# Kernel optimization log

Measured on AMD Instinct MI355X. Metric: run time of the kernel, lower is better.

## Reference

```python
import jax, jax.numpy as jnp
import numpy as np

EPS = 1e-5


def _layer(x, g, b, W_in, b_in, W_h, b_h, W_out, b_out):
    # x: [B, T, D]
    mu = jnp.mean(x, axis=-1, keepdims=True)
    var = jnp.mean(jnp.square(x - mu), axis=-1, keepdims=True)
    x_n = (x - mu) * jax.lax.rsqrt(var + EPS) * g + b
    # in_proj for all timesteps at once (same math as per-step linear)
    uv = jnp.einsum('btd,ed->bte', x_n, W_in) + b_in  # [B, T, 2D]
    d = x.shape[-1]
    u = jnp.transpose(uv[..., :d], (1, 0, 2))  # [T, B, D]
    v = jnp.transpose(uv[..., d:], (1, 0, 2))  # [T, B, D]

    def step(h, uv_t):
        u_t, v_t = uv_t
        gate = jax.nn.sigmoid(u_t)
        cand = jnp.tanh(v_t + h @ W_h.T + b_h)
        h_new = gate * cand + (1.0 - gate) * h
        y = h_new @ W_out.T + b_out
        return h_new, y

    h0 = jnp.zeros((x.shape[0], d), dtype=x.dtype)
    _, ys = jax.lax.scan(step, h0, (u, v))  # ys: [T, B, D]
    return x + jnp.transpose(ys, (1, 0, 2))


def setup_inputs() -> dict:
    key = jax.random.key(0)
    B, T, D, L = 8, 2048, 1024, 2
    ks = jax.random.split(key, 8)
    s = 1.0 / np.sqrt(D)
    return {
        'x': jax.random.normal(ks[0], (B, T, D), dtype=jnp.float32),
        'ln_g': jnp.ones((L, D), dtype=jnp.float32),
        'ln_b': jnp.zeros((L, D), dtype=jnp.float32),
        'W_in': jax.random.normal(ks[1], (L, 2 * D, D), dtype=jnp.float32) * s,
        'b_in': jnp.zeros((L, 2 * D), dtype=jnp.float32),
        'W_h': jax.random.normal(ks[2], (L, D, D), dtype=jnp.float32) * s,
        'b_h': jnp.zeros((L, D), dtype=jnp.float32),
        'W_out': jax.random.normal(ks[3], (L, D, D), dtype=jnp.float32) * s,
        'b_out': jnp.zeros((L, D), dtype=jnp.float32),
    }


def reference(x, ln_g, ln_b, W_in, b_in, W_h, b_h, W_out, b_out):
    out = x
    for l in range(W_in.shape[0]):  # small fixed n_layers loop
        out = _layer(out, ln_g[l], ln_b[l], W_in[l], b_in[l], W_h[l], b_h[l],
                     W_out[l], b_out[l])
    return out
```

## Files before the change

kernel.cpp:

```cpp
#include <hip/hip_runtime.h>
#include <stdint.h>
#include <stddef.h>

typedef __bf16 bf16;
typedef __bf16 bf16x8 __attribute__((ext_vector_type(8)));
typedef __bf16 bf16x4 __attribute__((ext_vector_type(4)));
typedef float  f32x4  __attribute__((ext_vector_type(4)));

#define B_ 8
#define T_ 2048
#define D_ 1024
#define L_ 2

#define AS1C(p) ((const __attribute__((address_space(1))) void*)(p))
#define AS3(p)  ((__attribute__((address_space(3))) void*)(p))


__global__ __launch_bounds__(256) void cvt_kernel(const float* __restrict__ in,
                                                  bf16* __restrict__ out, int n4) {
  int i = blockIdx.x * 256 + threadIdx.x;
  if (i >= n4) return;
  float4 v = ((const float4*)in)[i];
  bf16x4 o = { (bf16)v.x, (bf16)v.y, (bf16)v.z, (bf16)v.w };
  ((bf16x4*)out)[i] = o;
}

__global__ __launch_bounds__(256) void ln_kernel(const float* __restrict__ x,
                                                 const float* __restrict__ g,
                                                 const float* __restrict__ b,
                                                 bf16* __restrict__ xn) {
  const int row = blockIdx.x;
  const int tid = threadIdx.x;
  const float4 v = ((const float4*)(x + (size_t)row * D_))[tid];
  float s1 = v.x + v.y + v.z + v.w;
  float s2 = v.x * v.x + v.y * v.y + v.z * v.z + v.w * v.w;
#pragma unroll
  for (int off = 1; off < 64; off <<= 1) {
    s1 += __shfl_xor(s1, off);
    s2 += __shfl_xor(s2, off);
  }
  __shared__ float r1[4], r2[4];
  if ((tid & 63) == 0) { r1[tid >> 6] = s1; r2[tid >> 6] = s2; }
  __syncthreads();
  s1 = r1[0] + r1[1] + r1[2] + r1[3];
  s2 = r2[0] + r2[1] + r2[2] + r2[3];
  const float mu = s1 * (1.f / D_);
  const float var = s2 * (1.f / D_) - mu * mu;
  const float rs = rsqrtf(var + 1e-5f);
  const float4 gv = ((const float4*)g)[tid];
  const float4 bv = ((const float4*)b)[tid];
  bf16x4 o = { (bf16)((v.x - mu) * rs * gv.x + bv.x),
               (bf16)((v.y - mu) * rs * gv.y + bv.y),
               (bf16)((v.z - mu) * rs * gv.z + bv.z),
               (bf16)((v.w - mu) * rs * gv.w + bv.w) };
  ((bf16x4*)(xn + (size_t)row * D_))[tid] = o;
}

__global__ __launch_bounds__(256) void prep2_kernel(const float* __restrict__ Win2,
    const float* __restrict__ g2, const float* __restrict__ be2,
    const float* __restrict__ bin2, bf16* __restrict__ W2p,
    float* __restrict__ csum, float* __restrict__ cbias) {
  const int n = blockIdx.x;
  const int tid = threadIdx.x;
  const float4 w4 = ((const float4*)(Win2 + (size_t)n * 1024))[tid];
  const float4 g4 = ((const float4*)g2)[tid];
  const float4 b4 = ((const float4*)be2)[tid];
  bf16x4 o = { (bf16)(g4.x * w4.x), (bf16)(g4.y * w4.y),
               (bf16)(g4.z * w4.z), (bf16)(g4.w * w4.w) };
  ((bf16x4*)(W2p + (size_t)n * 1024))[tid] = o;
  float s = (float)o[0] + (float)o[1] + (float)o[2] + (float)o[3];
  float cbv = b4.x * w4.x + b4.y * w4.y + b4.z * w4.z + b4.w * w4.w;
#pragma unroll
  for (int off = 1; off < 64; off <<= 1) {
    s += __shfl_xor(s, off);
    cbv += __shfl_xor(cbv, off);
  }
  __shared__ float rs_[4], rc_[4];
  if ((tid & 63) == 0) { rs_[tid >> 6] = s; rc_[tid >> 6] = cbv; }
  __syncthreads();
  if (tid == 0) {
    csum[n] = rs_[0] + rs_[1] + rs_[2] + rs_[3];
    cbias[n] = rc_[0] + rc_[1] + rc_[2] + rc_[3] + bin2[n];
  }
}

__global__ __launch_bounds__(256) void gemm_uv(const bf16* __restrict__ A,
                                               const bf16* __restrict__ Bw,
                                               const float* __restrict__ bias,
                                               bf16* __restrict__ uvp,
                                               int M, int N, int K) {
  __shared__ bf16 As[128 * 32];
  __shared__ bf16 Bs[128 * 32];
  const int tid = threadIdx.x;
  const int lane = tid & 63;
  const int wave = tid >> 6;
  const int m0 = blockIdx.y * 128;
  const int n0 = blockIdx.x * 128;
  const int wm = (wave >> 1) * 64;
  const int wn = (wave & 1) * 64;
  f32x4 acc[4][4] = {};

  for (int kt = 0; kt < K; kt += 32) {
#pragma unroll
    for (int it = 0; it < 2; ++it) {
      const int gidx = it * 256 + tid;
      const int row = gidx >> 2;
      const int col = (gidx & 3) << 3;
      __builtin_amdgcn_global_load_lds(AS1C(A + (size_t)(m0 + row) * K + kt + col),
                                       AS3(&As[gidx * 8]), 16, 0, 0);
      __builtin_amdgcn_global_load_lds(AS1C(Bw + (size_t)(n0 + row) * K + kt + col),
                                       AS3(&Bs[gidx * 8]), 16, 0, 0);
    }
    __syncthreads();
    bf16x8 af[4], bfr[4];
#pragma unroll
    for (int i = 0; i < 4; ++i)
      af[i] = *(const bf16x8*)&As[(wm + i * 16 + (lane & 15)) * 32 + (lane >> 4) * 8];
#pragma unroll
    for (int j = 0; j < 4; ++j)
      bfr[j] = *(const bf16x8*)&Bs[(wn + j * 16 + (lane & 15)) * 32 + (lane >> 4) * 8];
#pragma unroll
    for (int i = 0; i < 4; ++i)
#pragma unroll
      for (int j = 0; j < 4; ++j)
        acc[i][j] = __builtin_amdgcn_mfma_f32_16x16x32_bf16(af[i], bfr[j], acc[i][j], 0, 0, 0);
    __syncthreads();
  }

  const int cr = (lane >> 4) * 4;
  const int cc = lane & 15;
#pragma unroll
  for (int i = 0; i < 4; ++i) {
#pragma unroll
    for (int j = 0; j < 4; ++j) {
      const int mb = m0 + wm + i * 16 + cr;
      const int n = n0 + wn + j * 16 + cc;
      const float bn = bias[n];
      const int p = n >> 10;
      const int nn2 = n & 1023;
#pragma unroll
      for (int r = 0; r < 4; ++r) {
        const int row = mb + r;
        const int b = row >> 11;
        const int t = row & (T_ - 1);
        uvp[(size_t)p * T_ * 8192 + (size_t)t * 8192 + nn2 * 8 + b] =
            (bf16)(acc[i][j][r] + bn);
      }
    }
  }
}

__global__ __launch_bounds__(256) void gemm_hfrag(const char* __restrict__ Hb,
                                                  const bf16* __restrict__ Bw,
                                                  const float* __restrict__ bias,
                                                  const char* __restrict__ residF,
                                                  float* __restrict__ C,
                                                  int M, int N, int K) {
  __shared__ bf16 As[128 * 32];
  __shared__ bf16 Bs[128 * 32];
  const int tid = threadIdx.x;
  const int lane = tid & 63;
  const int wave = tid >> 6;
  const int m0 = blockIdx.y * 128;
  const int n0 = blockIdx.x * 128;
  const int wm = (wave >> 1) * 64;
  const int wn = (wave & 1) * 64;
  f32x4 acc[4][4] = {};

  for (int kt = 0; kt < K; kt += 32) {
#pragma unroll
    for (int it = 0; it < 2; ++it) {
      const int g = it * 256 + tid;
      const int r = g >> 2;
      const int sub = g & 3;
      const int R = m0 + r;
      const int bb = R >> 11;
      const int tt = R & (T_ - 1);
      const char* src = Hb + (size_t)tt * 16384 + (size_t)(kt >> 5) * 512
                        + (sub * 8 + bb) * 16;
      __builtin_amdgcn_global_load_lds(AS1C(src), AS3(&As[g * 8]), 16, 0, 0);
      __builtin_amdgcn_global_load_lds(AS1C(Bw + (size_t)(n0 + r) * K + kt + (sub << 3)),
                                       AS3(&Bs[g * 8]), 16, 0, 0);
    }
    __syncthreads();
    bf16x8 af[4], bfr[4];
#pragma unroll
    for (int i = 0; i < 4; ++i)
      af[i] = *(const bf16x8*)&As[(wm + i * 16 + (lane & 15)) * 32 + (lane >> 4) * 8];
#pragma unroll
    for (int j = 0; j < 4; ++j)
      bfr[j] = *(const bf16x8*)&Bs[(wn + j * 16 + (lane & 15)) * 32 + (lane >> 4) * 8];
#pragma unroll
    for (int i = 0; i < 4; ++i)
#pragma unroll
      for (int j = 0; j < 4; ++j)
        acc[i][j] = __builtin_amdgcn_mfma_f32_16x16x32_bf16(af[i], bfr[j], acc[i][j], 0, 0, 0);
    __syncthreads();
  }

  const int cr = (lane >> 4) * 4;
  const int cc = lane & 15;
#pragma unroll
  for (int i = 0; i < 4; ++i) {
#pragma unroll
    for (int j = 0; j < 4; ++j) {
      const int mb = m0 + wm + i * 16 + cr;
      const int n = n0 + wn + j * 16 + cc;
      const float bn = bias[n];
      const int foffn = (n >> 5) * 512 + (((n & 31) >> 3) * 8) * 16 + (n & 7) * 2;
#pragma unroll
      for (int r = 0; r < 4; ++r) {
        const int row = mb + r;
        const int b = row >> 11;
        const int tt2 = row & (T_ - 1);
        const float resid =
            (float)*(const bf16*)(residF + (size_t)tt2 * 16384 + foffn + b * 16);
        C[(size_t)row * N + n] = acc[i][j][r] + bn + resid;
      }
    }
  }
}

__device__ __forceinline__ void load_wb(bf16x8 (&wB)[32], const bf16* Wrow) {
  const int half = ((threadIdx.x & 63) >> 4) << 3;
#pragma unroll
  for (int kk = 0; kk < 32; ++kk)
    wB[kk] = *(const bf16x8*)(Wrow + kk * 32 + half);
#pragma unroll
  for (int kk = 0; kk < 32; ++kk)
    asm volatile("" : "+a"(wB[kk]));
}

__device__ __forceinline__ f32x4 frag_matvec(const char* __restrict__ dF, int rdoff,
                                             const bf16x8 (&wB)[32]) {
  f32x4 a0 = {0.f, 0.f, 0.f, 0.f}, a1 = a0, a2 = a0, a3 = a0;
#pragma unroll
  for (int kk = 0; kk < 32; kk += 4) {
    bf16x8 f0 = *(const bf16x8*)(dF + kk * 512 + rdoff);
    bf16x8 f1 = *(const bf16x8*)(dF + (kk + 1) * 512 + rdoff);
    bf16x8 f2 = *(const bf16x8*)(dF + (kk + 2) * 512 + rdoff);
    bf16x8 f3 = *(const bf16x8*)(dF + (kk + 3) * 512 + rdoff);
    a0 = __builtin_amdgcn_mfma_f32_16x16x32_bf16(f0, wB[kk], a0, 0, 0, 0);
    a1 = __builtin_amdgcn_mfma_f32_16x16x32_bf16(f1, wB[kk + 1], a1, 0, 0, 0);
    a2 = __builtin_amdgcn_mfma_f32_16x16x32_bf16(f2, wB[kk + 2], a2, 0, 0, 0);
    a3 = __builtin_amdgcn_mfma_f32_16x16x32_bf16(f3, wB[kk + 3], a3, 0, 0, 0);
  }
  return (a0 + a1) + (a2 + a3);
}

template <int SLP>
__device__ __forceinline__ void poll8(const unsigned* base, unsigned tgt) {
  const int lane = threadIdx.x & 63;
  unsigned sv = tgt;
  if (lane < 8)
    sv = __hip_atomic_load(base + lane * 16, __ATOMIC_RELAXED, __HIP_MEMORY_SCOPE_AGENT);
  while (!__all((int)(sv >= tgt))) {
    __builtin_amdgcn_s_sleep(SLP);
    if (lane < 8)
      sv = __hip_atomic_load(base + lane * 16, __ATOMIC_RELAXED, __HIP_MEMORY_SCOPE_AGENT);
  }
  (void)__hip_atomic_load(base, __ATOMIC_ACQUIRE, __HIP_MEMORY_SCOPE_AGENT);
}

__device__ __forceinline__ void poll2s3(const unsigned* sync, int wg, unsigned tgt) {
  const int lane = threadIdx.x & 63;
  unsigned sv = tgt;
  if (lane < 2)
    sv = __hip_atomic_load(sync + 256 + ((lane ? 8 : 0) + wg) * 16,
                           __ATOMIC_RELAXED, __HIP_MEMORY_SCOPE_AGENT);
  while (!__all((int)(sv >= tgt))) {
    __builtin_amdgcn_s_sleep(1);
    if (lane < 2)
      sv = __hip_atomic_load(sync + 256 + ((lane ? 8 : 0) + wg) * 16,
                             __ATOMIC_RELAXED, __HIP_MEMORY_SCOPE_AGENT);
  }
  (void)__hip_atomic_load(sync + 256, __ATOMIC_ACQUIRE, __HIP_MEMORY_SCOPE_AGENT);
}

__device__ __forceinline__ void stage16k(const char* srcF, char* dstF, int tid) {
  __builtin_amdgcn_global_load_lds(AS1C(srcF + tid * 16), AS3(dstF + tid * 16), 16, 0, 0);
  __builtin_amdgcn_global_load_lds(AS1C(srcF + (512 + tid) * 16),
                                   AS3(dstF + (512 + tid) * 16), 16, 0, 0);
}

template <bool GATED>
__device__ __forceinline__ void scan_gang(int wg, const bf16* uvU, const bf16* uvV,
    const bf16* Wh, const float* bh, char* Hb, unsigned* sync, int ownBase,
    char (*hC)[16384], char (*tscr)[256]) {
  const int tid = threadIdx.x;
  const int lane = tid & 63;
  const int wv = tid >> 6;
  const int Wg = wg * 8 + wv;
  const int n0 = Wg * 16;
  const int c = lane & 15;

  bf16x8 wB[32];
  load_wb(wB, Wh + ((size_t)(n0 + c) << 10));

  const float bh_n = bh[n0 + c];
  const int b0 = (lane >> 4) * 4;
  const int rdoff = ((lane >> 4) * 8 + (lane & 7)) * 16;
  const int wregion = Wg * 256;

  float hs0 = 0.f, hs1 = 0.f, hs2 = 0.f, hs3 = 0.f;

  for (int t = 0; t < T_; ++t) {
    f32x4 asum = {0.f, 0.f, 0.f, 0.f};
    bf16x4 uq = {}, vq = {};
    if (t > 0) {
      poll8<1>(sync + ownBase, (unsigned)t);
      __builtin_amdgcn_sched_barrier(0);
      stage16k(Hb + (size_t)(t - 1) * 16384, hC[t & 1], tid);
      if (GATED) poll2s3(sync, wg, (unsigned)(t + 1));
      if (lane < 32) {
        uq = *(const bf16x4*)(uvU + (size_t)t * 8192 + (n0 + c) * 8 + b0);
        vq = *(const bf16x4*)(uvV + (size_t)t * 8192 + (n0 + c) * 8 + b0);
      }
      __syncthreads();
      asum = frag_matvec(hC[t & 1], rdoff, wB);
    } else {
      if (GATED) poll2s3(sync, wg, 1u);
      if (lane < 32) {
        uq = *(const bf16x4*)(uvU + (n0 + c) * 8 + b0);
        vq = *(const bf16x4*)(uvV + (n0 + c) * 8 + b0);
      }
    }

    char* wscr = tscr[wv];
    if (lane < 32) {
#pragma unroll
      for (int r = 0; r < 4; ++r) {
        const float uu = (float)uq[r];
        const float vv = (float)vq[r];
        float& hh = (r == 0) ? hs0 : (r == 1) ? hs1 : (r == 2) ? hs2 : hs3;
        const float s = asum[r] + bh_n + vv;
        const float gg = __builtin_amdgcn_rcpf(1.f + __expf(-uu));
        const float e = __expf(2.f * s);
        const float cand = 1.f - 2.f * __builtin_amdgcn_rcpf(e + 1.f);
        hh = fmaf(gg, cand - hh, hh);
        *(bf16*)(wscr + (c >> 3) * 128 + (b0 + r) * 16 + (c & 7) * 2) = (bf16)hh;
      }
    }
    asm volatile("s_waitcnt lgkmcnt(0)" ::: "memory");
    __builtin_amdgcn_sched_barrier(0);
    if (lane < 32) {
      const unsigned long long pv = *(const unsigned long long*)(wscr + lane * 8);
      char* dst = Hb + (size_t)t * 16384 + wregion + lane * 8;
      __hip_atomic_store((unsigned long long*)dst, pv,
                         __ATOMIC_RELAXED, __HIP_MEMORY_SCOPE_AGENT);
    }
    __syncthreads();
    if (tid == 0)
      __hip_atomic_store(sync + ownBase + wg * 16, (unsigned)(t + 1),
                         __ATOMIC_RELEASE, __HIP_MEMORY_SCOPE_AGENT);
    __builtin_amdgcn_sched_barrier(0);
  }
}

__device__ __forceinline__ void s2_gang(int wg, const char* H1, const bf16* Wout,
    const float* bout, const float* x, char* out1F, unsigned* sync,
    char (*hC)[16384], char (*tscr)[256]) {
  const int tid = threadIdx.x;
  const int lane = tid & 63;
  const int wv = tid >> 6;
  const int W2 = wg * 8 + wv;
  const int n0 = W2 * 16;
  const int c = lane & 15;

  bf16x8 wB[32];
  load_wb(wB, Wout + ((size_t)(n0 + c) << 10));

  const float bo = bout[n0 + c];
  const int b0 = (lane >> 4) * 4;
  const int rdoff = ((lane >> 4) * 8 + (lane & 7)) * 16;
  const int wregion = W2 * 256;

  f32x4 xq = {0.f, 0.f, 0.f, 0.f};
  if (lane < 32) {
#pragma unroll
    for (int r = 0; r < 4; ++r)
      xq[r] = x[((size_t)(b0 + r) * T_) * 1024 + n0 + c];
  }

  poll8<4>(sync, 1u);
  __builtin_amdgcn_sched_barrier(0);
  stage16k(H1, hC[0], tid);

  for (int t = 0; t < T_; ++t) {
    __syncthreads();
    f32x4 asum = frag_matvec(hC[t & 1], rdoff, wB);

    char* wscr = tscr[wv];
    if (lane < 32) {
#pragma unroll
      for (int r = 0; r < 4; ++r) {
        const float o = xq[r] + asum[r] + bo;
        *(bf16*)(wscr + (c >> 3) * 128 + (b0 + r) * 16 + (c & 7) * 2) = (bf16)o;
      }
    }
    asm volatile("s_waitcnt lgkmcnt(0)" ::: "memory");
    __builtin_amdgcn_sched_barrier(0);
    if (lane < 32) {
      const unsigned long long pv = *(const unsigned long long*)(wscr + lane * 8);
      char* dst = out1F + (size_t)t * 16384 + wregion + lane * 8;
      __hip_atomic_store((unsigned long long*)dst, pv,
                         __ATOMIC_RELAXED, __HIP_MEMORY_SCOPE_AGENT);
    }
    __syncthreads();
    if (tid == 0)
      __hip_atomic_store(sync + 128 + wg * 16, (unsigned)(t + 1),
                         __ATOMIC_RELEASE, __HIP_MEMORY_SCOPE_AGENT);
    __builtin_amdgcn_sched_barrier(0);
    if (t + 1 < T_) {
      poll8<4>(sync, (unsigned)(t + 2));
      __builtin_amdgcn_sched_barrier(0);
      stage16k(H1 + (size_t)(t + 1) * 16384, hC[(t + 1) & 1], tid);
      if (lane < 32) {
#pragma unroll
        for (int r = 0; r < 4; ++r)
          xq[r] = x[((size_t)(b0 + r) * T_ + (t + 1)) * 1024 + n0 + c];
      }
    }
  }
}

__device__ __forceinline__ void s3_gang(int wg, const char* out1F, const bf16* W2p,
    const float* csum2, const float* cbias2, bf16* uv2, unsigned* sync,
    char (*hC)[16384], char (*tscr)[256], float* statp) {
  const int tid = threadIdx.x;
  const int lane = tid & 63;
  const int wv = tid >> 6;
  const int W3 = wg * 8 + wv;
  const int c = lane & 15;
  const int n = W3 * 16 + c;

  bf16x8 wB[32];
  load_wb(wB, W2p + ((size_t)n << 10));

  const float cs = csum2[n];
  const float cb = cbias2[n];
  const int b0 = (lane >> 4) * 4;
  const int rdoff = ((lane >> 4) * 8 + (lane & 7)) * 16;
  char* outPlane = (char*)(uv2 + (size_t)(W3 >> 6) * T_ * 8192);
  const int nn = (W3 & 63) * 16;
  const int sidx = wv * 128 + lane;

  poll8<4>(sync + 128, 1u);
  __builtin_amdgcn_sched_barrier(0);
  stage16k(out1F, hC[0], tid);

  for (int t = 0; t < T_; ++t) {
    __syncthreads();
    const char* dstF = hC[t & 1];
    {
      bf16x8 v0 = *(const bf16x8*)(dstF + sidx * 16);
      bf16x8 v1 = *(const bf16x8*)(dstF + sidx * 16 + 1024);
      float s1 = 0.f, s2 = 0.f;
#pragma unroll
      for (int j = 0; j < 8; ++j) {
        const float f0 = (float)v0[j], f1 = (float)v1[j];
        s1 += f0 + f1;
        s2 += f0 * f0 + f1 * f1;
      }
#pragma unroll
      for (int off = 8; off < 64; off <<= 1) {
        s1 += __shfl_xor(s1, off);
        s2 += __shfl_xor(s2, off);
      }
      if (lane < 8) {
        statp[(wv * 8 + lane) * 2] = s1;
        statp[(wv * 8 + lane) * 2 + 1] = s2;
      }
    }
    f32x4 asum = frag_matvec(dstF, rdoff, wB);
    __syncthreads();
    char* wscr = tscr[wv];
    if (lane < 32) {
#pragma unroll
      for (int r = 0; r < 4; ++r) {
        const int b = b0 + r;
        float s1 = 0.f, s2 = 0.f;
#pragma unroll
        for (int w = 0; w < 8; ++w) {
          s1 += statp[(w * 8 + b) * 2];
          s2 += statp[(w * 8 + b) * 2 + 1];
        }
        const float mu = s1 * (1.f / 1024.f);
        const float var = s2 * (1.f / 1024.f) - mu * mu;
        const float rs = rsqrtf(var + 1e-5f);
        const float val = rs * (asum[r] - mu * cs) + cb;
        *(bf16*)(wscr + c * 16 + b * 2) = (bf16)val;
      }
    }
    asm volatile("s_waitcnt lgkmcnt(0)" ::: "memory");
    __builtin_amdgcn_sched_barrier(0);
    if (lane < 32) {
      const unsigned long long pv = *(const unsigned long long*)(wscr + lane * 8);
      char* dst = outPlane + (size_t)t * 16384 + nn * 16 + lane * 8;
      __hip_atomic_store((unsigned long long*)dst, pv,
                         __ATOMIC_RELAXED, __HIP_MEMORY_SCOPE_AGENT);
    }
    __syncthreads();
    if (tid == 0)
      __hip_atomic_store(sync + 256 + wg * 16, (unsigned)(t + 1),
                         __ATOMIC_RELEASE, __HIP_MEMORY_SCOPE_AGENT);
    __builtin_amdgcn_sched_barrier(0);
    if (t + 1 < T_) {
      poll8<4>(sync + 128, (unsigned)(t + 2));
      __builtin_amdgcn_sched_barrier(0);
      stage16k(out1F + (size_t)(t + 1) * 16384, hC[(t + 1) & 1], tid);
    }
  }
}

__global__ __launch_bounds__(512, 1) void mega_kernel(
    const bf16* __restrict__ uv1, const bf16* __restrict__ Wh,
    const float* __restrict__ bh, const bf16* __restrict__ Wout,
    const float* __restrict__ bout, const float* __restrict__ x,
    const bf16* __restrict__ W2p, const float* __restrict__ csum2,
    const float* __restrict__ cbias2, char* __restrict__ H1,
    char* __restrict__ out1F, bf16* __restrict__ uv2, char* __restrict__ H2,
    unsigned* __restrict__ sync) {
  __shared__ __align__(16) char hC[2][16384];
  __shared__ __align__(16) char tscr[8][256];
  __shared__ float statp[128];
  const int bid = blockIdx.x;
  if (bid < 8) {
    scan_gang<false>(bid, uv1, uv1 + (size_t)T_ * 8192, Wh, bh, H1, sync, 0, hC, tscr);
  } else if (bid < 16) {
    s2_gang(bid - 8, H1, Wout, bout, x, out1F, sync, hC, tscr);
  } else if (bid < 32) {
    s3_gang(bid - 16, out1F, W2p, csum2, cbias2, uv2, sync, hC, tscr, statp);
  } else {
    scan_gang<true>(bid - 32, uv2, uv2 + (size_t)T_ * 8192,
                    Wh + (size_t)D_ * D_, bh + D_, H2, sync, 512, hC, tscr);
  }
}

extern "C" void kernel_launch(void* const* d_in, const int* in_sizes, int n_in,
                              void* d_out, int out_size, void* d_ws, size_t ws_size,
                              hipStream_t stream) {
  const float* x     = (const float*)d_in[0];
  const float* ln_g  = (const float*)d_in[1];
  const float* ln_b  = (const float*)d_in[2];
  const float* W_in  = (const float*)d_in[3];
  const float* b_in  = (const float*)d_in[4];
  const float* W_h   = (const float*)d_in[5];
  const float* b_h   = (const float*)d_in[6];
  const float* W_out = (const float*)d_in[7];
  const float* b_out = (const float*)d_in[8];
  float* out = (float*)d_out;

  char* ws = (char*)d_ws;
  size_t off = 0;
  auto alloc = [&](size_t bytes) -> void* {
    void* p = ws + off;
    off = (off + bytes + 255) & ~(size_t)255;
    return p;
  };
  bf16* wInB   = (bf16*)alloc((size_t)L_ * 2 * D_ * D_ * 2);
  bf16* wHB    = (bf16*)alloc((size_t)L_ * D_ * D_ * 2);
  bf16* wOutB  = (bf16*)alloc((size_t)L_ * D_ * D_ * 2);
  bf16* W2p    = (bf16*)alloc((size_t)2 * D_ * D_ * 2);
  float* csum2 = (float*)alloc(2 * D_ * 4);
  float* cbias2= (float*)alloc(2 * D_ * 4);
  bf16* Xn     = (bf16*)alloc((size_t)B_ * T_ * D_ * 2);
  char* H2     = (char*)Xn;
  bf16* uvp1   = (bf16*)alloc((size_t)2 * T_ * 8192 * 2);
  char* H1     = (char*)alloc((size_t)T_ * 16384);
  char* out1F  = (char*)alloc((size_t)T_ * 16384);
  bf16* uvp2   = (bf16*)alloc((size_t)2 * T_ * 8192 * 2);
  unsigned* sync = (unsigned*)alloc(4096);
  (void)ws_size; (void)in_sizes; (void)n_in; (void)out_size;

  {
    int n4 = L_ * 2 * D_ * D_ / 4;
    cvt_kernel<<<(n4 + 255) / 256, 256, 0, stream>>>(W_in, wInB, n4);
    n4 = L_ * D_ * D_ / 4;
    cvt_kernel<<<(n4 + 255) / 256, 256, 0, stream>>>(W_h, wHB, n4);
    cvt_kernel<<<(n4 + 255) / 256, 256, 0, stream>>>(W_out, wOutB, n4);
  }
  prep2_kernel<<<2 * D_, 256, 0, stream>>>(W_in + (size_t)2 * D_ * D_,
                                           ln_g + D_, ln_b + D_, b_in + 2 * D_,
                                           W2p, csum2, cbias2);

  const int Mrows = B_ * T_;
  ln_kernel<<<Mrows, 256, 0, stream>>>(x, ln_g, ln_b, Xn);

  dim3 g1(2 * D_ / 128, Mrows / 128);
  gemm_uv<<<g1, 256, 0, stream>>>(Xn, wInB, b_in, uvp1, Mrows, 2 * D_, D_);

  (void)hipMemsetAsync(sync, 0, 4096, stream);
  mega_kernel<<<40, 512, 0, stream>>>(uvp1, wHB, b_h, wOutB, b_out, x,
                                      W2p, csum2, cbias2, H1, out1F, uvp2, H2, sync);

  dim3 g2(D_ / 128, Mrows / 128);
  gemm_hfrag<<<g2, 256, 0, stream>>>(H2, wOutB + (size_t)D_ * D_, b_out + D_,
                                     out1F, out, Mrows, D_, D_);
}
```

Before: 11.64 ms.

## Merge scan polls and prefetch next-step u/v gate inputs with lookahead gating

Merges the own-gang step poll and the stage-3 gate poll into one wave-wide poll loop over up to 10 lanes. The gate target becomes t+8 rather than t+1, so the in-projection producer must run eight steps ahead. The next timestep's u/v values are now loaded right after the sync store, taking that global load off the critical path of the serial recurrence. The risk is extra waiting whenever the producer is not a full eight steps ahead.

Result: faster. 9.388 ms (-19.3%).

```diff
diff --git a/kernel.cpp b/kernel.cpp
--- a/kernel.cpp
+++ b/kernel.cpp
@@ -262,19 +262,23 @@
   (void)__hip_atomic_load(base, __ATOMIC_ACQUIRE, __HIP_MEMORY_SCOPE_AGENT);
 }
 
-__device__ __forceinline__ void poll2s3(const unsigned* sync, int wg, unsigned tgt) {
+template <bool GATED>
+__device__ __forceinline__ void poll_comb(const unsigned* sync, int ownBase, int wg,
+                                          unsigned tOwn, unsigned tGate) {
   const int lane = threadIdx.x & 63;
-  unsigned sv = tgt;
-  if (lane < 2)
-    sv = __hip_atomic_load(sync + 256 + ((lane ? 8 : 0) + wg) * 16,
-                           __ATOMIC_RELAXED, __HIP_MEMORY_SCOPE_AGENT);
+  const unsigned* addr = sync + ownBase;
+  unsigned tgt = 0u;
+  if (lane < 8) { addr = sync + ownBase + lane * 16; tgt = tOwn; }
+  else if (GATED && lane < 10) {
+    addr = sync + 256 + ((lane == 9 ? 8 : 0) + wg) * 16;
+    tgt = tGate;
+  }
+  unsigned sv = __hip_atomic_load(addr, __ATOMIC_RELAXED, __HIP_MEMORY_SCOPE_AGENT);
   while (!__all((int)(sv >= tgt))) {
     __builtin_amdgcn_s_sleep(1);
-    if (lane < 2)
-      sv = __hip_atomic_load(sync + 256 + ((lane ? 8 : 0) + wg) * 16,
-                             __ATOMIC_RELAXED, __HIP_MEMORY_SCOPE_AGENT);
-  }
-  (void)__hip_atomic_load(sync + 256, __ATOMIC_ACQUIRE, __HIP_MEMORY_SCOPE_AGENT);
+    sv = __hip_atomic_load(addr, __ATOMIC_RELAXED, __HIP_MEMORY_SCOPE_AGENT);
+  }
+  (void)__hip_atomic_load(sync + ownBase, __ATOMIC_ACQUIRE, __HIP_MEMORY_SCOPE_AGENT);
 }
 
 __device__ __forceinline__ void stage16k(const char* srcF, char* dstF, int tid) {
@@ -303,27 +307,23 @@
   const int wregion = Wg * 256;
 
   float hs0 = 0.f, hs1 = 0.f, hs2 = 0.f, hs3 = 0.f;
+  bf16x4 uq = {}, vq = {};
+
+  if (GATED) poll_comb<true>(sync, ownBase, wg, 0u, (unsigned)(8 < T_ ? 8 : T_));
+  if (lane < 32) {
+    uq = *(const bf16x4*)(uvU + (n0 + c) * 8 + b0);
+    vq = *(const bf16x4*)(uvV + (n0 + c) * 8 + b0);
+  }
 
   for (int t = 0; t < T_; ++t) {
     f32x4 asum = {0.f, 0.f, 0.f, 0.f};
-    bf16x4 uq = {}, vq = {};
     if (t > 0) {
-      poll8<1>(sync + ownBase, (unsigned)t);
+      const unsigned g = (unsigned)((t + 8 < T_) ? t + 8 : T_);
+      poll_comb<GATED>(sync, ownBase, wg, (unsigned)t, g);
       __builtin_amdgcn_sched_barrier(0);
       stage16k(Hb + (size_t)(t - 1) * 16384, hC[t & 1], tid);
-      if (GATED) poll2s3(sync, wg, (unsigned)(t + 1));
-      if (lane < 32) {
-        uq = *(const bf16x4*)(uvU + (size_t)t * 8192 + (n0 + c) * 8 + b0);
-        vq = *(const bf16x4*)(uvV + (size_t)t * 8192 + (n0 + c) * 8 + b0);
-      }
       __syncthreads();
       asum = frag_matvec(hC[t & 1], rdoff, wB);
-    } else {
-      if (GATED) poll2s3(sync, wg, 1u);
-      if (lane < 32) {
-        uq = *(const bf16x4*)(uvU + (n0 + c) * 8 + b0);
-        vq = *(const bf16x4*)(uvV + (n0 + c) * 8 + b0);
-      }
     }
 
     char* wscr = tscr[wv];
@@ -354,6 +354,10 @@
       __hip_atomic_store(sync + ownBase + wg * 16, (unsigned)(t + 1),
                          __ATOMIC_RELEASE, __HIP_MEMORY_SCOPE_AGENT);
     __builtin_amdgcn_sched_barrier(0);
+    if (t < T_ - 1 && lane < 32) {
+      uq = *(const bf16x4*)(uvU + (size_t)(t + 1) * 8192 + (n0 + c) * 8 + b0);
+      vq = *(const bf16x4*)(uvV + (size_t)(t + 1) * 8192 + (n0 + c) * 8 + b0);
+    }
   }
 }
 
```

## Use per-wave step flags and batch cross-gang polling in recurrent scan

Applied to the files above, without the earlier changes.

The recurrent stage now publishes a per-wave progress flag right after each wave's h slice is stored, which removes the block-wide barrier before signaling. Consumers poll 64 per-wave flags with one load per lane instead of 8 per-block flags. The gating poll on the stage-3 producer now runs only every 8 steps, with a lookahead of 15, and the next step's u/v loads are issued early so they overlap the wait. This cuts per-timestep latency on the serial critical path. In exchange it adds more flag traffic and depends on the sync buffer layout matching the new indexing.

After: 14.84 ms. +27.5%, slower.

```diff
diff --git a/kernel.cpp b/kernel.cpp
--- a/kernel.cpp
+++ b/kernel.cpp
@@ -249,7 +249,18 @@
 }
 
 template <int SLP>
-__device__ __forceinline__ void poll8(const unsigned* base, unsigned tgt) {
+__device__ __forceinline__ void poll64(const unsigned* base, unsigned tgt) {
+  const int lane = threadIdx.x & 63;
+  unsigned sv = __hip_atomic_load(base + lane, __ATOMIC_RELAXED, __HIP_MEMORY_SCOPE_AGENT);
+  while (!__all((int)(sv >= tgt))) {
+    __builtin_amdgcn_s_sleep(SLP);
+    sv = __hip_atomic_load(base + lane, __ATOMIC_RELAXED, __HIP_MEMORY_SCOPE_AGENT);
+  }
+  (void)__hip_atomic_load(base, __ATOMIC_ACQUIRE, __HIP_MEMORY_SCOPE_AGENT);
+}
+
+template <int SLP>
+__device__ __forceinline__ void poll8p(const unsigned* base, unsigned tgt) {
   const int lane = threadIdx.x & 63;
   unsigned sv = tgt;
   if (lane < 8)
@@ -303,27 +314,24 @@
   const int wregion = Wg * 256;
 
   float hs0 = 0.f, hs1 = 0.f, hs2 = 0.f, hs3 = 0.f;
+  bf16x4 uq = {}, vq = {};
+
+  if (GATED) poll2s3(sync, wg, (unsigned)(16 < T_ ? 16 : T_));
+  if (lane < 32) {
+    uq = *(const bf16x4*)(uvU + (n0 + c) * 8 + b0);
+    vq = *(const bf16x4*)(uvV + (n0 + c) * 8 + b0);
+  }
 
   for (int t = 0; t < T_; ++t) {
     f32x4 asum = {0.f, 0.f, 0.f, 0.f};
-    bf16x4 uq = {}, vq = {};
     if (t > 0) {
-      poll8<1>(sync + ownBase, (unsigned)t);
+      poll64<1>(sync + ownBase, (unsigned)t);
       __builtin_amdgcn_sched_barrier(0);
       stage16k(Hb + (size_t)(t - 1) * 16384, hC[t & 1], tid);
-      if (GATED) poll2s3(sync, wg, (unsigned)(t + 1));
-      if (lane < 32) {
-        uq = *(const bf16x4*)(uvU + (size_t)t * 8192 + (n0 + c) * 8 + b0);
-        vq = *(const bf16x4*)(uvV + (size_t)t * 8192 + (n0 + c) * 8 + b0);
-      }
+      if (GATED && (t & 7) == 1)
+        poll2s3(sync, wg, (unsigned)((t + 15 < T_) ? t + 15 : T_));
       __syncthreads();
       asum = frag_matvec(hC[t & 1], rdoff, wB);
-    } else {
-      if (GATED) poll2s3(sync, wg, 1u);
-      if (lane < 32) {
-        uq = *(const bf16x4*)(uvU + (n0 + c) * 8 + b0);
-        vq = *(const bf16x4*)(uvV + (n0 + c) * 8 + b0);
-      }
     }
 
     char* wscr = tscr[wv];
@@ -349,11 +357,14 @@
       __hip_atomic_store((unsigned long long*)dst, pv,
                          __ATOMIC_RELAXED, __HIP_MEMORY_SCOPE_AGENT);
     }
-    __syncthreads();
-    if (tid == 0)
-      __hip_atomic_store(sync + ownBase + wg * 16, (unsigned)(t + 1),
+    if (lane == 0)
+      __hip_atomic_store(sync + ownBase + Wg, (unsigned)(t + 1),
                          __ATOMIC_RELEASE, __HIP_MEMORY_SCOPE_AGENT);
     __builtin_amdgcn_sched_barrier(0);
+    if (t < T_ - 1 && lane < 32) {
+      uq = *(const bf16x4*)(uvU + (size_t)(t + 1) * 8192 + (n0 + c) * 8 + b0);
+      vq = *(const bf16x4*)(uvV + (size_t)(t + 1) * 8192 + (n0 + c) * 8 + b0);
+    }
   }
 }
 
@@ -382,7 +393,7 @@
       xq[r] = x[((size_t)(b0 + r) * T_) * 1024 + n0 + c];
   }
 
-  poll8<4>(sync, 1u);
+  poll64<4>(sync, 1u);
   __builtin_amdgcn_sched_barrier(0);
   stage16k(H1, hC[0], tid);
 
@@ -412,7 +423,7 @@
                          __ATOMIC_RELEASE, __HIP_MEMORY_SCOPE_AGENT);
     __builtin_amdgcn_sched_barrier(0);
     if (t + 1 < T_) {
-      poll8<4>(sync, (unsigned)(t + 2));
+      poll64<4>(sync, (unsigned)(t + 2));
       __builtin_amdgcn_sched_barrier(0);
       stage16k(H1 + (size_t)(t + 1) * 16384, hC[(t + 1) & 1], tid);
       if (lane < 32) {
@@ -445,7 +456,7 @@
   const int nn = (W3 & 63) * 16;
   const int sidx = wv * 128 + lane;
 
-  poll8<4>(sync + 128, 1u);
+  poll8p<4>(sync + 128, 1u);
   __builtin_amdgcn_sched_barrier(0);
   stage16k(out1F, hC[0], tid);
 
@@ -506,7 +517,7 @@
                          __ATOMIC_RELEASE, __HIP_MEMORY_SCOPE_AGENT);
     __builtin_amdgcn_sched_barrier(0);
     if (t + 1 < T_) {
-      poll8<4>(sync + 128, (unsigned)(t + 2));
+      poll8p<4>(sync + 128, (unsigned)(t + 2));
       __builtin_amdgcn_sched_barrier(0);
       stage16k(out1F + (size_t)(t + 1) * 16384, hC[(t + 1) & 1], tid);
     }
```
